# Optimization experiments

Hardware: AMD Instinct MI355X
Metric: run time of the kernel (lower is better)

The kernel has to match this reference:

```python
import jax, jax.numpy as jnp
import numpy as np

B, I, H = 2048, 512, 512


def _hamilton_matrix(W):
    """W: [4, O, Iin] quaternion weight components (r,i,j,k).
    Returns real block matrix M: [4*Iin, 4*O] implementing the Hamilton
    product W (*) x for component-major flattened input [r|i|j|k]."""
    Wr, Wi, Wj, Wk = W[0].T, W[1].T, W[2].T, W[3].T  # each [Iin, O]
    row_r = jnp.concatenate([Wr, Wi, Wj, Wk], axis=1)
    row_i = jnp.concatenate([-Wi, Wr, Wk, -Wj], axis=1)
    row_j = jnp.concatenate([-Wj, -Wk, Wr, Wi], axis=1)
    row_k = jnp.concatenate([-Wk, Wj, -Wi, Wr], axis=1)
    return jnp.concatenate([row_r, row_i, row_j, row_k], axis=0)


def qlinear(x, W, b=None):
    """x: [B, Iin, 4]; W: [4, O, Iin]; b: [O, 4] or None -> [B, O, 4]."""
    Bn, Iin, _ = x.shape
    O = W.shape[1]
    xf = x.transpose(0, 2, 1).reshape(Bn, 4 * Iin)  # component-major flatten
    out = xf @ _hamilton_matrix(W)                   # [B, 4*O]
    out = out.reshape(Bn, 4, O).transpose(0, 2, 1)   # [B, O, 4]
    if b is not None:
        out = out + b
    return out


def setup_inputs() -> dict:
    key = jax.random.key(0)
    ks = jax.random.split(key, 16)
    s_in = 0.02   # weight scale for numerical sanity
    d = {
        "x": jax.random.normal(ks[0], (B, I, 4), jnp.float32),
        "h": jax.random.normal(ks[1], (B, H, 4), jnp.float32),
        "c": jax.random.normal(ks[2], (B, H, 4), jnp.float32),
        "Wi_w": jax.random.normal(ks[3], (4, H, I), jnp.float32) * s_in,
        "Wf_w": jax.random.normal(ks[4], (4, H, I), jnp.float32) * s_in,
        "Wo_w": jax.random.normal(ks[5], (4, H, I), jnp.float32) * s_in,
        "Wc_w": jax.random.normal(ks[6], (4, H, I), jnp.float32) * s_in,
        "Ui_w": jax.random.normal(ks[7], (4, H, H), jnp.float32) * s_in,
        "Uf_w": jax.random.normal(ks[8], (4, H, H), jnp.float32) * s_in,
        "Uo_w": jax.random.normal(ks[9], (4, H, H), jnp.float32) * s_in,
        "Uc_w": jax.random.normal(ks[10], (4, H, H), jnp.float32) * s_in,
        "Ui_b": jax.random.normal(ks[11], (H, 4), jnp.float32) * s_in,
        "Uf_b": jax.random.normal(ks[12], (H, 4), jnp.float32) * s_in,
        "Uo_b": jax.random.normal(ks[13], (H, 4), jnp.float32) * s_in,
        "Uc_b": jax.random.normal(ks[14], (H, 4), jnp.float32) * s_in,
    }
    return d


def reference(x, h, c, Wi_w, Wf_w, Wo_w, Wc_w, Ui_w, Uf_w, Uo_w, Uc_w,
              Ui_b, Uf_b, Uo_b, Uc_b):
    # Scalar gates from real (index-0) component of quaternion gate preacts.
    i_pre = qlinear(x, Wi_w) + qlinear(h, Ui_w, Ui_b)
    f_pre = qlinear(x, Wf_w) + qlinear(h, Uf_w, Uf_b)
    o_pre = qlinear(x, Wo_w) + qlinear(h, Uo_w, Uo_b)
    c_tilde = jnp.tanh(qlinear(x, Wc_w) + qlinear(h, Uc_w, Uc_b))
    i = jax.nn.sigmoid(i_pre[..., 0])[..., None]  # [B, H, 1] broadcasts over 4 comps
    f = jax.nn.sigmoid(f_pre[..., 0])[..., None]
    o = jax.nn.sigmoid(o_pre[..., 0])[..., None]
    c_t = f * c + i * c_tilde
    h_t = o * jnp.tanh(c_t)
    return (h_t, c_t)
```

## Files before the change

kernel.cpp:

```cpp
#include <hip/hip_runtime.h>
#include <hip/hip_bf16.h>


#define BDIM 256
#define GDIM 512

typedef __attribute__((ext_vector_type(8))) short short8;
typedef __attribute__((ext_vector_type(4))) float f32x4;

typedef const __attribute__((address_space(1))) void* gptr_t;
typedef __attribute__((address_space(3))) void* lptr_t;

__device__ __forceinline__ ushort f2b(float f) {
  __hip_bfloat16 h = __float2bfloat16(f);
  union { __hip_bfloat16 b; ushort u; } cv;
  cv.b = h;
  return cv.u;
}

__global__ __launch_bounds__(BDIM) void pack_kernel(
    const float* __restrict__ x, const float* __restrict__ h,
    const float* __restrict__ w0, const float* __restrict__ w1,
    const float* __restrict__ w2, const float* __restrict__ w3,
    const float* __restrict__ u0, const float* __restrict__ u1,
    const float* __restrict__ u2, const float* __restrict__ u3,
    ushort* __restrict__ A, ushort* __restrict__ Wp) {
  if (blockIdx.x < 2048) {
    int tid = blockIdx.x * BDIM + threadIdx.x;
    int b = tid >> 8;
    int pos0 = (tid & 255) << 2;
    const float* src = (pos0 < 512)
        ? (x + ((size_t)b * 512 + pos0) * 4)
        : (h + ((size_t)b * 512 + (pos0 - 512)) * 4);
    float4 q0 = reinterpret_cast<const float4*>(src)[0];
    float4 q1 = reinterpret_cast<const float4*>(src)[1];
    float4 q2 = reinterpret_cast<const float4*>(src)[2];
    float4 q3 = reinterpret_cast<const float4*>(src)[3];
    int swz = (b & 7) << 3;
    ushort* Ab = A + (size_t)b * 4096 + (pos0 ^ swz);
    union { ushort u[4]; uint2 v; } r0, r1, r2, r3;
    r0.u[0] = f2b(q0.x); r0.u[1] = f2b(q1.x); r0.u[2] = f2b(q2.x); r0.u[3] = f2b(q3.x);
    r1.u[0] = f2b(q0.y); r1.u[1] = f2b(q1.y); r1.u[2] = f2b(q2.y); r1.u[3] = f2b(q3.y);
    r2.u[0] = f2b(q0.z); r2.u[1] = f2b(q1.z); r2.u[2] = f2b(q2.z); r2.u[3] = f2b(q3.z);
    r3.u[0] = f2b(q0.w); r3.u[1] = f2b(q1.w); r3.u[2] = f2b(q2.w); r3.u[3] = f2b(q3.w);
    *reinterpret_cast<uint2*>(Ab)        = r0.v;
    *reinterpret_cast<uint2*>(Ab + 1024) = r1.v;
    *reinterpret_cast<uint2*>(Ab + 2048) = r2.v;
    *reinterpret_cast<uint2*>(Ab + 3072) = r3.v;
  } else {
    int tid = (blockIdx.x - 2048) * BDIM + threadIdx.x;
    int n = tid >> 9;
    int k = (tid & 511) << 3;
    int swz = (n & 7) << 3;
    ushort* dst = Wp + (size_t)n * 4096 + (k ^ swz);
    int o = n >> 3, g = n & 7;
    if (g == 7) {
      uint4 z = {0u, 0u, 0u, 0u};
      *reinterpret_cast<uint4*>(dst) = z;
      return;
    }
    int cin = k >> 10, pos = k & 1023;
    int part = pos >> 9, ii = pos & 511;
    int gi = (g < 3) ? g : 3;
    int co = (g < 3) ? 0 : g - 3;
    int comp = cin ^ co;
    float sg = ((0x5390u >> ((cin << 2) | co)) & 1u) ? -1.0f : 1.0f;
    const float* base;
    if (part == 0) base = (gi == 0) ? w0 : (gi == 1) ? w1 : (gi == 2) ? w2 : w3;
    else           base = (gi == 0) ? u0 : (gi == 1) ? u1 : (gi == 2) ? u2 : u3;
    const float* p = base + (size_t)comp * 262144 + (size_t)o * 512 + ii;
    float4 v0 = *reinterpret_cast<const float4*>(p);
    float4 v1 = *reinterpret_cast<const float4*>(p + 4);
    union { ushort u[8]; uint4 v; } r;
    r.u[0] = f2b(sg * v0.x); r.u[1] = f2b(sg * v0.y);
    r.u[2] = f2b(sg * v0.z); r.u[3] = f2b(sg * v0.w);
    r.u[4] = f2b(sg * v1.x); r.u[5] = f2b(sg * v1.y);
    r.u[6] = f2b(sg * v1.z); r.u[7] = f2b(sg * v1.w);
    *reinterpret_cast<uint4*>(dst) = r.v;
  }
}

__global__ __launch_bounds__(GDIM, 2) void gemm_cell_kernel(
    const ushort* __restrict__ A, const ushort* __restrict__ Wp,
    const float* __restrict__ cin_, const float* __restrict__ bi,
    const float* __restrict__ bfg, const float* __restrict__ bo,
    const float* __restrict__ bc, float* __restrict__ out) {
  __shared__ ushort SMEM[73728];
  ushort* As = SMEM;
  ushort* Bs = SMEM + 24576;

  const int t = threadIdx.x;
  const int lane = t & 63;
  const int wid = t >> 6;
  const int wm = wid >> 2;
  const int wn = wid & 3;
  const int lrow = lane & 15;
  const int lk8 = (lane >> 4) << 3;
  const int swzE = (lrow & 7) << 3;

  const int bid = blockIdx.x;
  const int xcd = bid & 7;
  const int loc = bid >> 3;
  const int bx = (xcd & 1) * 8 + (loc & 7);
  const int by = (xcd >> 1) * 4 + (loc >> 3);
  const int m0 = by * 128;
  const int n0 = bx * 256;

  f32x4 acc[4][4];
#pragma unroll
  for (int mi = 0; mi < 4; ++mi)
#pragma unroll
    for (int ni = 0; ni < 4; ++ni)
      acc[mi][ni] = (f32x4){0.f, 0.f, 0.f, 0.f};

  const ushort* Ag = A + (size_t)m0 * 4096;
  const ushort* Bg = Wp + (size_t)n0 * 4096;
  const int c8 = (t & 7) << 3;

#define STAGE_A(KT, S, I)                                                     \
  {                                                                           \
    int j = t + (I) * 512;                                                    \
    __builtin_amdgcn_global_load_lds(                                         \
        (gptr_t)(Ag + (size_t)(j >> 3) * 4096 + (KT) * 64 + c8),              \
        (lptr_t)(As + (S) * 8192 + j * 8), 16, 0, 0);                         \
  }
#define STAGE_B(KT, S, I)                                                     \
  {                                                                           \
    int j = t + (I) * 512;                                                    \
    __builtin_amdgcn_global_load_lds(                                         \
        (gptr_t)(Bg + (size_t)(j >> 3) * 4096 + (KT) * 64 + c8),              \
        (lptr_t)(Bs + (S) * 16384 + j * 8), 16, 0, 0);                        \
  }

  STAGE_A(0, 0, 0) STAGE_A(0, 0, 1)
  STAGE_B(0, 0, 0) STAGE_B(0, 0, 1) STAGE_B(0, 0, 2) STAGE_B(0, 0, 3)
  STAGE_A(1, 1, 0) STAGE_A(1, 1, 1)
  STAGE_B(1, 1, 0) STAGE_B(1, 1, 1) STAGE_B(1, 1, 2) STAGE_B(1, 1, 3)
  asm volatile("s_waitcnt vmcnt(6)" ::: "memory");
  __builtin_amdgcn_s_barrier();
  __builtin_amdgcn_sched_barrier(0);

  int cur = 0;
  for (int kt = 0; kt < 64; ++kt) {
    const int pf = (kt < 62);
    const int ps = (cur >= 1) ? cur - 1 : 2;
    const ushort* Ac = As + cur * 8192;
    const ushort* Bc = Bs + cur * 16384;

    {
      const int c0 = lk8 ^ swzE;
      short8 af[4], bf[4];
#pragma unroll
      for (int mi = 0; mi < 4; ++mi)
        af[mi] = *reinterpret_cast<const short8*>(Ac + (wm * 64 + mi * 16 + lrow) * 64 + c0);
#pragma unroll
      for (int ni = 0; ni < 4; ++ni)
        bf[ni] = *reinterpret_cast<const short8*>(Bc + (wn * 64 + ni * 16 + lrow) * 64 + c0);
      if (pf) { STAGE_A(kt + 2, ps, 0) STAGE_A(kt + 2, ps, 1) STAGE_B(kt + 2, ps, 0) }
      __builtin_amdgcn_s_setprio(1);
#pragma unroll
      for (int mi = 0; mi < 4; ++mi)
#pragma unroll
        for (int ni = 0; ni < 4; ++ni)
          acc[mi][ni] = __builtin_amdgcn_mfma_f32_16x16x32_bf16(
              af[mi], bf[ni], acc[mi][ni], 0, 0, 0);
      __builtin_amdgcn_s_setprio(0);
    }
    {
      const int c1 = (32 + lk8) ^ swzE;
      short8 af[4], bf[4];
#pragma unroll
      for (int mi = 0; mi < 4; ++mi)
        af[mi] = *reinterpret_cast<const short8*>(Ac + (wm * 64 + mi * 16 + lrow) * 64 + c1);
#pragma unroll
      for (int ni = 0; ni < 4; ++ni)
        bf[ni] = *reinterpret_cast<const short8*>(Bc + (wn * 64 + ni * 16 + lrow) * 64 + c1);
      if (pf) { STAGE_B(kt + 2, ps, 1) STAGE_B(kt + 2, ps, 2) STAGE_B(kt + 2, ps, 3) }
      __builtin_amdgcn_s_setprio(1);
#pragma unroll
      for (int mi = 0; mi < 4; ++mi)
#pragma unroll
        for (int ni = 0; ni < 4; ++ni)
          acc[mi][ni] = __builtin_amdgcn_mfma_f32_16x16x32_bf16(
              af[mi], bf[ni], acc[mi][ni], 0, 0, 0);
      __builtin_amdgcn_s_setprio(0);
    }

    if (kt < 62)       { asm volatile("s_waitcnt vmcnt(6)" ::: "memory"); }
    else if (kt == 62) { asm volatile("s_waitcnt vmcnt(0)" ::: "memory"); }
    __builtin_amdgcn_s_barrier();
    __builtin_amdgcn_sched_barrier(0);
    cur = (cur == 2) ? 0 : cur + 1;
  }
  __syncthreads();

  float* Es = (float*)SMEM;
  const int o0 = bx * 32;
  const int lr4 = (lane >> 4) << 2;

#pragma unroll
  for (int wmc = 0; wmc < 2; ++wmc) {
#pragma unroll
    for (int mi = 0; mi < 4; ++mi) {
      if (wm == wmc) {
#pragma unroll
        for (int ni = 0; ni < 4; ++ni) {
          float* dst = Es + lr4 * 260 + wn * 64 + ni * 16 + lrow;
#pragma unroll
          for (int r = 0; r < 4; ++r) dst[r * 260] = acc[mi][ni][r];
        }
      }
      __syncthreads();
      {
        int bl = t >> 5;
        int ol = t & 31;
        const float* e = Es + bl * 260 + ol * 8;
        int b = m0 + wmc * 64 + mi * 16 + bl;
        int o = o0 + ol;
        float4 bcv = *reinterpret_cast<const float4*>(bc + (size_t)o * 4);
        float ip = e[0] + bi[o << 2];
        float fp = e[1] + bfg[o << 2];
        float op = e[2] + bo[o << 2];
        float g0 = tanhf(e[3] + bcv.x);
        float g1 = tanhf(e[4] + bcv.y);
        float g2 = tanhf(e[5] + bcv.z);
        float g3 = tanhf(e[6] + bcv.w);
        float ig = 1.f / (1.f + expf(-ip));
        float fg = 1.f / (1.f + expf(-fp));
        float og = 1.f / (1.f + expf(-op));
        float4 cv = *reinterpret_cast<const float4*>(cin_ + ((size_t)b * 512 + o) * 4);
        float4 ct, ht;
        ct.x = fg * cv.x + ig * g0;  ht.x = og * tanhf(ct.x);
        ct.y = fg * cv.y + ig * g1;  ht.y = og * tanhf(ct.y);
        ct.z = fg * cv.z + ig * g2;  ht.z = og * tanhf(ct.z);
        ct.w = fg * cv.w + ig * g3;  ht.w = og * tanhf(ct.w);
        *reinterpret_cast<float4*>(out + ((size_t)b * 512 + o) * 4) = ht;
        *reinterpret_cast<float4*>(out + 4194304 + ((size_t)b * 512 + o) * 4) = ct;
      }
      __syncthreads();
    }
  }
#undef STAGE_A
#undef STAGE_B
}

extern "C" void kernel_launch(void* const* d_in, const int* in_sizes, int n_in,
                              void* d_out, int out_size, void* d_ws, size_t ws_size,
                              hipStream_t stream) {
  const float* x   = (const float*)d_in[0];
  const float* h   = (const float*)d_in[1];
  const float* c   = (const float*)d_in[2];
  const float* wi  = (const float*)d_in[3];
  const float* wf  = (const float*)d_in[4];
  const float* wo  = (const float*)d_in[5];
  const float* wc  = (const float*)d_in[6];
  const float* ui  = (const float*)d_in[7];
  const float* uf  = (const float*)d_in[8];
  const float* uo  = (const float*)d_in[9];
  const float* uc  = (const float*)d_in[10];
  const float* bi  = (const float*)d_in[11];
  const float* bf_ = (const float*)d_in[12];
  const float* bo  = (const float*)d_in[13];
  const float* bc  = (const float*)d_in[14];
  float* out = (float*)d_out;

  ushort* A  = (ushort*)d_ws;
  ushort* Wp = (ushort*)((char*)d_ws + (size_t)16777216);

  hipLaunchKernelGGL(pack_kernel, dim3(10240), dim3(BDIM), 0, stream,
                     x, h, wi, wf, wo, wc, ui, uf, uo, uc, A, Wp);
  hipLaunchKernelGGL(gemm_cell_kernel, dim3(256), dim3(GDIM), 0, stream,
                     A, Wp, c, bi, bf_, bo, bc, out);
}
```

Baseline: 214.3 us.

## Split GEMM k-step into four barrier-synchronized phases interleaving LDS reads, prefetch, MFMA

After: 222.4 us. 1.04x slower.

```diff
diff --git a/kernel.cpp b/kernel.cpp
--- a/kernel.cpp
+++ b/kernel.cpp
@@ -131,6 +131,16 @@
         (gptr_t)(Bg + (size_t)(j >> 3) * 4096 + (KT) * 64 + c8),              \
         (lptr_t)(Bs + (S) * 16384 + j * 8), 16, 0, 0);                        \
   }
+#define LDA(MI, CC) (*reinterpret_cast<const short8*>(                        \
+    Ac + (wm * 64 + (MI) * 16 + lrow) * 64 + (CC)))
+#define LDB(NI, CC) (*reinterpret_cast<const short8*>(                        \
+    Bc + (wn * 64 + (NI) * 16 + lrow) * 64 + (CC)))
+#define MFMA(AV, BV, ACC)                                                     \
+  ACC = __builtin_amdgcn_mfma_f32_16x16x32_bf16((AV), (BV), (ACC), 0, 0, 0);
+#define PHASE_SYNC()                                                          \
+  __builtin_amdgcn_s_barrier();                                               \
+  asm volatile("s_waitcnt lgkmcnt(0)" ::: "memory");                          \
+  __builtin_amdgcn_sched_barrier(0);
 
   STAGE_A(0, 0, 0) STAGE_A(0, 0, 1)
   STAGE_B(0, 0, 0) STAGE_B(0, 0, 1) STAGE_B(0, 0, 2) STAGE_B(0, 0, 3)
@@ -146,46 +156,54 @@
     const int ps = (cur >= 1) ? cur - 1 : 2;
     const ushort* Ac = As + cur * 8192;
     const ushort* Bc = Bs + cur * 16384;
-
-    {
-      const int c0 = lk8 ^ swzE;
-      short8 af[4], bf[4];
-#pragma unroll
-      for (int mi = 0; mi < 4; ++mi)
-        af[mi] = *reinterpret_cast<const short8*>(Ac + (wm * 64 + mi * 16 + lrow) * 64 + c0);
-#pragma unroll
-      for (int ni = 0; ni < 4; ++ni)
-        bf[ni] = *reinterpret_cast<const short8*>(Bc + (wn * 64 + ni * 16 + lrow) * 64 + c0);
-      if (pf) { STAGE_A(kt + 2, ps, 0) STAGE_A(kt + 2, ps, 1) STAGE_B(kt + 2, ps, 0) }
-      __builtin_amdgcn_s_setprio(1);
-#pragma unroll
-      for (int mi = 0; mi < 4; ++mi)
-#pragma unroll
-        for (int ni = 0; ni < 4; ++ni)
-          acc[mi][ni] = __builtin_amdgcn_mfma_f32_16x16x32_bf16(
-              af[mi], bf[ni], acc[mi][ni], 0, 0, 0);
-      __builtin_amdgcn_s_setprio(0);
-    }
-    {
-      const int c1 = (32 + lk8) ^ swzE;
-      short8 af[4], bf[4];
-#pragma unroll
-      for (int mi = 0; mi < 4; ++mi)
-        af[mi] = *reinterpret_cast<const short8*>(Ac + (wm * 64 + mi * 16 + lrow) * 64 + c1);
-#pragma unroll
-      for (int ni = 0; ni < 4; ++ni)
-        bf[ni] = *reinterpret_cast<const short8*>(Bc + (wn * 64 + ni * 16 + lrow) * 64 + c1);
-      if (pf) { STAGE_B(kt + 2, ps, 1) STAGE_B(kt + 2, ps, 2) STAGE_B(kt + 2, ps, 3) }
-      __builtin_amdgcn_s_setprio(1);
-#pragma unroll
-      for (int mi = 0; mi < 4; ++mi)
-#pragma unroll
-        for (int ni = 0; ni < 4; ++ni)
-          acc[mi][ni] = __builtin_amdgcn_mfma_f32_16x16x32_bf16(
-              af[mi], bf[ni], acc[mi][ni], 0, 0, 0);
-      __builtin_amdgcn_s_setprio(0);
-    }
-
+    const int c0 = lk8 ^ swzE;
+    const int c1 = (32 + lk8) ^ swzE;
+    short8 a0, a1, a2, a3, b0, b1, b2, b3;
+
+    a0 = LDA(0, c0); a1 = LDA(1, c0); a2 = LDA(2, c0); a3 = LDA(3, c0);
+    b0 = LDB(0, c0); b1 = LDB(1, c0);
+    if (pf) { STAGE_A(kt + 2, ps, 0) STAGE_A(kt + 2, ps, 1) }
+    PHASE_SYNC();
+    __builtin_amdgcn_s_setprio(1);
+    MFMA(a0, b0, acc[0][0]) MFMA(a1, b0, acc[1][0])
+    MFMA(a2, b0, acc[2][0]) MFMA(a3, b0, acc[3][0])
+    MFMA(a0, b1, acc[0][1]) MFMA(a1, b1, acc[1][1])
+    MFMA(a2, b1, acc[2][1]) MFMA(a3, b1, acc[3][1])
+    __builtin_amdgcn_s_setprio(0);
+    __builtin_amdgcn_s_barrier();
+
+    b2 = LDB(2, c0); b3 = LDB(3, c0);
+    if (pf) { STAGE_B(kt + 2, ps, 0) STAGE_B(kt + 2, ps, 1) }
+    PHASE_SYNC();
+    __builtin_amdgcn_s_setprio(1);
+    MFMA(a0, b2, acc[0][2]) MFMA(a1, b2, acc[1][2])
+    MFMA(a2, b2, acc[2][2]) MFMA(a3, b2, acc[3][2])
+    MFMA(a0, b3, acc[0][3]) MFMA(a1, b3, acc[1][3])
+    MFMA(a2, b3, acc[2][3]) MFMA(a3, b3, acc[3][3])
+    __builtin_amdgcn_s_setprio(0);
+    __builtin_amdgcn_s_barrier();
+
+    a0 = LDA(0, c1); a1 = LDA(1, c1); a2 = LDA(2, c1); a3 = LDA(3, c1);
+    b0 = LDB(0, c1); b1 = LDB(1, c1);
+    if (pf) { STAGE_B(kt + 2, ps, 2) }
+    PHASE_SYNC();
+    __builtin_amdgcn_s_setprio(1);
+    MFMA(a0, b0, acc[0][0]) MFMA(a1, b0, acc[1][0])
+    MFMA(a2, b0, acc[2][0]) MFMA(a3, b0, acc[3][0])
+    MFMA(a0, b1, acc[0][1]) MFMA(a1, b1, acc[1][1])
+    MFMA(a2, b1, acc[2][1]) MFMA(a3, b1, acc[3][1])
+    __builtin_amdgcn_s_setprio(0);
+    __builtin_amdgcn_s_barrier();
+
+    b2 = LDB(2, c1); b3 = LDB(3, c1);
+    if (pf) { STAGE_B(kt + 2, ps, 3) }
+    PHASE_SYNC();
+    __builtin_amdgcn_s_setprio(1);
+    MFMA(a0, b2, acc[0][2]) MFMA(a1, b2, acc[1][2])
+    MFMA(a2, b2, acc[2][2]) MFMA(a3, b2, acc[3][2])
+    MFMA(a0, b3, acc[0][3]) MFMA(a1, b3, acc[1][3])
+    MFMA(a2, b3, acc[2][3]) MFMA(a3, b3, acc[3][3])
+    __builtin_amdgcn_s_setprio(0);
     if (kt < 62)       { asm volatile("s_waitcnt vmcnt(6)" ::: "memory"); }
     else if (kt == 62) { asm volatile("s_waitcnt vmcnt(0)" ::: "memory"); }
     __builtin_amdgcn_s_barrier();
@@ -242,6 +260,10 @@
   }
 #undef STAGE_A
 #undef STAGE_B
+#undef LDA
+#undef LDB
+#undef MFMA
+#undef PHASE_SYNC
 }
 
 extern "C" void kernel_launch(void* const* d_in, const int* in_sizes, int n_in,
```
